# Performance work log

Measured on AMD Instinct MI355X. Metric: run time of the kernel, lower is better.

## Reference

```python
import jax, jax.numpy as jnp
import numpy as np

B, H, K, E = 8, 256, 256, 128
VOCAB, FVOCAB = 30000, 1000


def setup_inputs() -> dict:
    key = jax.random.key(0)
    k1, k2, k3, k4, k5, k6 = jax.random.split(key, 6)
    key_emb = jax.random.normal(k2, (VOCAB, E), dtype=jnp.float32)
    value_emb = jax.random.normal(k3, (FVOCAB, E), dtype=jnp.float32)
    # padding_idx=0 rows are zero
    key_emb = key_emb.at[0].set(0.0)
    value_emb = value_emb.at[0].set(0.0)
    return {
        "hidden": jax.random.normal(k1, (B, H, E), dtype=jnp.float32),
        "key_emb": key_emb,
        "value_emb": value_emb,
        "key_seq": jax.random.randint(k4, (B, K), 0, VOCAB, dtype=jnp.int64) if jax.config.jax_enable_x64 else jax.random.randint(k4, (B, K), 0, VOCAB).astype(jnp.int32),
        "value_seq": jax.random.randint(k5, (B, H, K), 0, FVOCAB).astype(jnp.int32),
        "mask_matrix": jax.random.randint(k6, (B, H, K), 0, 2).astype(jnp.int32),
    }


def reference(hidden, key_emb, value_emb, key_seq, value_seq, mask_matrix):
    scale = jnp.asarray(np.power(E, 0.5), dtype=jnp.float32)
    # embedding gathers (padding_idx=0 -> zero row, enforced in setup)
    k = key_emb[key_seq]            # [B, K, E]
    v = value_emb[value_seq]        # [B, H, K, E]
    # masked exp-normalize attention (manual, not softmax: no max-subtract)
    u = jnp.einsum('bhe,bke->bhk', hidden, k) / scale   # [B, H, K]
    delta = jnp.exp(u) * mask_matrix.astype(jnp.float32)
    p = delta / (jnp.sum(delta, axis=2, keepdims=True) + 1e-10)  # [B, H, K]
    # attention-weighted value aggregation
    o = jnp.einsum('bhk,bhke->bhe', p, v)               # [B, H, E]
    # nonzero-count averaging over H
    aspect_len = jnp.sum(o != 0, axis=1).astype(jnp.float32)     # [B, E]
    avg_o = jnp.sum(o, axis=1) / aspect_len                      # [B, E]
    return avg_o
```

## Files before the change

kernel.cpp:

```cpp
#include <hip/hip_runtime.h>
#include <math.h>

#define BB 8
#define HH 256
#define KK 256
#define EE 128
#define HJ 4
#define NBLK (BB * HH / HJ)
#define NBIN 1024

template <int CTRL, int RM>
__device__ __forceinline__ float dpp_add(float x) {
    int d = __builtin_amdgcn_update_dpp(0, __float_as_int(x), CTRL, RM, 0xf, true);
    return x + __int_as_float(d);
}
__device__ __forceinline__ float dpp_reduce_half(float x) {
    x = dpp_add<0x111, 0xf>(x);
    x = dpp_add<0x112, 0xf>(x);
    x = dpp_add<0x114, 0xf>(x);
    x = dpp_add<0x118, 0xf>(x);
    x = dpp_add<0x142, 0xa>(x);
    return x;
}
__device__ __forceinline__ float dpp_reduce_wave(float x) {
    x = dpp_reduce_half(x);
    x = dpp_add<0x143, 0xc>(x);
    return x;
}

__global__ __launch_bounds__(256) void kvmn_attn_hist(
    const float* __restrict__ hidden,
    const float* __restrict__ key_emb,
    const int*   __restrict__ key_seq,
    const int*   __restrict__ value_seq,
    const int*   __restrict__ mask,
    float* __restrict__ part_hist,
    int*   __restrict__ c_part)
{
    __shared__ float sh_u[HJ][KK];
    __shared__ float hist[NBIN];
    __shared__ float fslot[HJ][4];
    __shared__ int   islot[HJ][4];

    const int bid  = blockIdx.x;
    const int b    = bid >> 6;
    const int h0   = (bid & 63) * HJ;
    const int tid  = threadIdx.x;
    const int w    = tid >> 6;
    const int lane = tid & 63;
    const int half = lane >> 5;
    const int sub  = lane & 31;

    const int ksreg = key_seq[b * KK + tid];

    float4 h4[HJ];
    #pragma unroll
    for (int j = 0; j < HJ; ++j)
        h4[j] = *(const float4*)&hidden[(size_t)(b * HH + h0 + j) * EE + sub * 4];

    *(float4*)&hist[tid * 4] = make_float4(0.f, 0.f, 0.f, 0.f);

    const float inv_scale = 0.08838834764831845f;

    #pragma unroll 8
    for (int i = 0; i < 32; ++i) {
        const int    row = __shfl(ksreg, half * 32 + i, 64);
        const float4 kv  = *(const float4*)&key_emb[(size_t)row * EE + sub * 4];
        const int    k2  = w * 64 + half * 32 + i;
        #pragma unroll
        for (int j = 0; j < HJ; ++j) {
            float part = kv.x * h4[j].x + kv.y * h4[j].y + kv.z * h4[j].z + kv.w * h4[j].w;
            part = dpp_reduce_half(part);
            if (sub == 31) sh_u[j][k2] = part * inv_scale;
        }
    }
    __syncthreads();

    float d[HJ];
    int   vs[HJ];
    #pragma unroll
    for (int j = 0; j < HJ; ++j) {
        const size_t idx = (size_t)(b * HH + h0 + j) * KK + tid;
        const int m = mask[idx];
        vs[j] = value_seq[idx];
        d[j]  = expf(sh_u[j][tid]) * (float)m;
        const float s = dpp_reduce_wave(d[j]);
        if (lane == 63) fslot[j][w] = s;
        const int any = __any(m != 0 && vs[j] != 0);
        if (lane == 0) islot[j][w] = any ? 1 : 0;
    }
    __syncthreads();

    #pragma unroll
    for (int j = 0; j < HJ; ++j) {
        const float denom = fslot[j][0] + fslot[j][1] + fslot[j][2] + fslot[j][3];
        const float p = d[j] * (1.0f / (denom + 1e-10f));
        atomicAdd(&hist[vs[j]], p);
    }
    if (tid == 0) {
        int c = 0;
        #pragma unroll
        for (int j = 0; j < HJ; ++j)
            c += (islot[j][0] | islot[j][1] | islot[j][2] | islot[j][3]);
        c_part[bid] = c;
    }
    __syncthreads();

    *(float4*)&part_hist[(size_t)bid * NBIN + tid * 4] = *(float4*)&hist[tid * 4];
}

__global__ __launch_bounds__(512) void kvmn_finalize(
    const float* __restrict__ part_hist,
    const int*   __restrict__ c_part,
    const float* __restrict__ value_emb,
    float* __restrict__ out)
{
    __shared__ float H[NBIN];
    __shared__ float gs[4][EE];
    __shared__ int   csh[64];
    __shared__ float cval;

    const int b   = blockIdx.x;
    const int tid = threadIdx.x;

    float2 acc2 = make_float2(0.f, 0.f);
    #pragma unroll 8
    for (int i = 0; i < 64; ++i) {
        const float2 v = *(const float2*)&part_hist[(size_t)(b * 64 + i) * NBIN + tid * 2];
        acc2.x += v.x;
        acc2.y += v.y;
    }
    *(float2*)&H[tid * 2] = acc2;
    if (tid < 64) csh[tid] = c_part[b * 64 + tid];
    __syncthreads();
    if (tid == 0) {
        int c = 0;
        #pragma unroll
        for (int i = 0; i < 64; ++i) c += csh[i];
        cval = (float)c;
    }

    const int e  = tid & 127;
    const int qt = tid >> 7;
    float acc = 0.f;
    const int bin0 = qt * 250;
    #pragma unroll 5
    for (int bin = bin0; bin < bin0 + 250; ++bin)
        acc += H[bin] * value_emb[(size_t)bin * EE + e];
    gs[qt][e] = acc;
    __syncthreads();
    if (tid < 128)
        out[b * EE + tid] = (gs[0][tid] + gs[1][tid] + gs[2][tid] + gs[3][tid]) / cval;
}

extern "C" void kernel_launch(void* const* d_in, const int* in_sizes, int n_in,
                              void* d_out, int out_size, void* d_ws, size_t ws_size,
                              hipStream_t stream) {
    const float* hidden    = (const float*)d_in[0];
    const float* key_emb   = (const float*)d_in[1];
    const float* value_emb = (const float*)d_in[2];
    const int*   key_seq   = (const int*)d_in[3];
    const int*   value_seq = (const int*)d_in[4];
    const int*   mask      = (const int*)d_in[5];

    float* part_hist = (float*)d_ws;
    int*   c_part    = (int*)((char*)d_ws + (size_t)NBLK * NBIN * 4);

    kvmn_attn_hist<<<NBLK, 256, 0, stream>>>(hidden, key_emb, key_seq,
                                             value_seq, mask, part_hist, c_part);
    kvmn_finalize<<<BB, 512, 0, stream>>>(part_hist, c_part, value_emb, (float*)d_out);
    (void)in_sizes; (void)n_in; (void)out_size; (void)ws_size;
}
```

Baseline: 115.5 us.

## Merge attention and finalize into one cooperative kernel with parallel reduction

Replaces the two-kernel pipeline with a single cooperative kernel of 1024 blocks, each handling 2 heads instead of 4. Grid syncs separate the phases. The histogram reduction and value-embedding projection are spread over 512 blocks, each taking a 16-bin chunk, instead of running on only 8 blocks. A final phase sums the partial outputs per batch. This targets the serial finalize tail and the launch gap between kernels. In exchange it adds two grid-wide barriers, doubles the partial-histogram traffic to 4 MB, and needs all blocks co-resident.

```diff
diff --git a/kernel.cpp b/kernel.cpp
--- a/kernel.cpp
+++ b/kernel.cpp
@@ -1,13 +1,18 @@
 #include <hip/hip_runtime.h>
+#include <hip/hip_cooperative_groups.h>
 #include <math.h>
+
+namespace cg = cooperative_groups;
 
 #define BB 8
 #define HH 256
 #define KK 256
 #define EE 128
-#define HJ 4
-#define NBLK (BB * HH / HJ)
 #define NBIN 1024
+#define GRID 1024
+#define BPB 128
+#define CHUNK 16
+#define NCH (NBIN / CHUNK)
 
 template <int CTRL, int RM>
 __device__ __forceinline__ float dpp_add(float x) {
@@ -28,129 +33,163 @@
     return x;
 }
 
-__global__ __launch_bounds__(256) void kvmn_attn_hist(
+__global__ __launch_bounds__(256, 4) void kvmn_coop(
     const float* __restrict__ hidden,
     const float* __restrict__ key_emb,
+    const float* __restrict__ value_emb,
     const int*   __restrict__ key_seq,
     const int*   __restrict__ value_seq,
     const int*   __restrict__ mask,
     float* __restrict__ part_hist,
-    int*   __restrict__ c_part)
+    float* __restrict__ partial_out,
+    int*   __restrict__ c_part,
+    float* __restrict__ out)
 {
-    __shared__ float sh_u[HJ][KK];
+    __shared__ float sh_u[2][KK];
     __shared__ float hist[NBIN];
-    __shared__ float fslot[HJ][4];
-    __shared__ int   islot[HJ][4];
+    __shared__ float fslot[2][4];
+    __shared__ int   islot[2][4];
+    __shared__ float red[CHUNK][17];
+    __shared__ float Hc[CHUNK];
+    __shared__ float gs[2][EE];
+    __shared__ int   sh_c[256];
+    __shared__ float sh_cf;
+
+    cg::grid_group grid = cg::this_grid();
 
     const int bid  = blockIdx.x;
-    const int b    = bid >> 6;
-    const int h0   = (bid & 63) * HJ;
     const int tid  = threadIdx.x;
     const int w    = tid >> 6;
     const int lane = tid & 63;
     const int half = lane >> 5;
     const int sub  = lane & 31;
 
-    const int ksreg = key_seq[b * KK + tid];
-
-    float4 h4[HJ];
-    #pragma unroll
-    for (int j = 0; j < HJ; ++j)
-        h4[j] = *(const float4*)&hidden[(size_t)(b * HH + h0 + j) * EE + sub * 4];
-
-    *(float4*)&hist[tid * 4] = make_float4(0.f, 0.f, 0.f, 0.f);
-
-    const float inv_scale = 0.08838834764831845f;
-
-    #pragma unroll 8
-    for (int i = 0; i < 32; ++i) {
-        const int    row = __shfl(ksreg, half * 32 + i, 64);
-        const float4 kv  = *(const float4*)&key_emb[(size_t)row * EE + sub * 4];
-        const int    k2  = w * 64 + half * 32 + i;
-        #pragma unroll
-        for (int j = 0; j < HJ; ++j) {
-            float part = kv.x * h4[j].x + kv.y * h4[j].y + kv.z * h4[j].z + kv.w * h4[j].w;
-            part = dpp_reduce_half(part);
-            if (sub == 31) sh_u[j][k2] = part * inv_scale;
-        }
+    {
+        const int b  = bid >> 7;
+        const int h0 = (bid * 2) & 255;
+
+        const int ksreg = key_seq[b * KK + tid];
+
+        float4 h4[2];
+        #pragma unroll
+        for (int j = 0; j < 2; ++j)
+            h4[j] = *(const float4*)&hidden[((size_t)b * HH + h0 + j) * EE + sub * 4];
+
+        *(float4*)&hist[tid * 4] = make_float4(0.f, 0.f, 0.f, 0.f);
+
+        const float inv_scale = 0.08838834764831845f;
+
+        #pragma unroll 8
+        for (int i = 0; i < 32; ++i) {
+            const int    row = __shfl(ksreg, half * 32 + i, 64);
+            const float4 kv  = *(const float4*)&key_emb[(size_t)row * EE + sub * 4];
+            const int    k2  = w * 64 + half * 32 + i;
+            float p0 = kv.x * h4[0].x + kv.y * h4[0].y + kv.z * h4[0].z + kv.w * h4[0].w;
+            float p1 = kv.x * h4[1].x + kv.y * h4[1].y + kv.z * h4[1].z + kv.w * h4[1].w;
+            p0 = dpp_reduce_half(p0);
+            p1 = dpp_reduce_half(p1);
+            if (sub == 31) {
+                sh_u[0][k2] = p0 * inv_scale;
+                sh_u[1][k2] = p1 * inv_scale;
+            }
+        }
+        __syncthreads();
+
+        float d[2];
+        int   vs[2];
+        #pragma unroll
+        for (int j = 0; j < 2; ++j) {
+            const size_t idx = ((size_t)b * HH + h0 + j) * KK + tid;
+            const int m = mask[idx];
+            vs[j] = value_seq[idx];
+            d[j]  = expf(sh_u[j][tid]) * (float)m;
+            const float s = dpp_reduce_wave(d[j]);
+            if (lane == 63) fslot[j][w] = s;
+            const unsigned long long bal = __ballot(m != 0 && vs[j] != 0);
+            if (lane == 0) islot[j][w] = (bal != 0ull) ? 1 : 0;
+        }
+        __syncthreads();
+
+        #pragma unroll
+        for (int j = 0; j < 2; ++j) {
+            const float denom = fslot[j][0] + fslot[j][1] + fslot[j][2] + fslot[j][3];
+            const float p = d[j] * (1.0f / (denom + 1e-10f));
+            atomicAdd(&hist[vs[j]], p);
+        }
+        if (tid == 0) {
+            const int f0 = islot[0][0] | islot[0][1] | islot[0][2] | islot[0][3];
+            const int f1 = islot[1][0] | islot[1][1] | islot[1][2] | islot[1][3];
+            c_part[bid] = f0 + f1;
+        }
+        __syncthreads();
+
+        *(float4*)&part_hist[(size_t)bid * NBIN + tid * 4] = *(float4*)&hist[tid * 4];
     }
-    __syncthreads();
-
-    float d[HJ];
-    int   vs[HJ];
-    #pragma unroll
-    for (int j = 0; j < HJ; ++j) {
-        const size_t idx = (size_t)(b * HH + h0 + j) * KK + tid;
-        const int m = mask[idx];
-        vs[j] = value_seq[idx];
-        d[j]  = expf(sh_u[j][tid]) * (float)m;
-        const float s = dpp_reduce_wave(d[j]);
-        if (lane == 63) fslot[j][w] = s;
-        const int any = __any(m != 0 && vs[j] != 0);
-        if (lane == 0) islot[j][w] = any ? 1 : 0;
+
+    __threadfence();
+    grid.sync();
+
+    if (bid < BB * NCH) {
+        const int b    = bid >> 6;
+        const int j    = bid & (NCH - 1);
+        const int bin0 = j * CHUNK;
+
+        const int bin = tid & 15;
+        const int rg  = tid >> 4;
+        float s = 0.0f;
+        const float* basep = part_hist + (size_t)(b * BPB + rg * 8) * NBIN + bin0 + bin;
+        #pragma unroll
+        for (int r = 0; r < 8; ++r)
+            s += basep[(size_t)r * NBIN];
+        red[bin][rg] = s;
+        __syncthreads();
+        if (tid < CHUNK) {
+            float t2 = 0.0f;
+            #pragma unroll
+            for (int g = 0; g < 16; ++g) t2 += red[tid][g];
+            Hc[tid] = t2;
+        }
+        __syncthreads();
+
+        const int e  = tid & 127;
+        const int hf = tid >> 7;
+        float acc = 0.0f;
+        #pragma unroll
+        for (int i = 0; i < 8; ++i) {
+            const int gb = bin0 + hf * 8 + i;
+            if (gb < 1000)
+                acc += Hc[hf * 8 + i] * value_emb[(size_t)gb * EE + e];
+        }
+        gs[hf][e] = acc;
+        __syncthreads();
+        if (tid < EE)
+            partial_out[((size_t)b * NCH + j) * EE + tid] = gs[0][tid] + gs[1][tid];
     }
-    __syncthreads();
-
-    #pragma unroll
-    for (int j = 0; j < HJ; ++j) {
-        const float denom = fslot[j][0] + fslot[j][1] + fslot[j][2] + fslot[j][3];
-        const float p = d[j] * (1.0f / (denom + 1e-10f));
-        atomicAdd(&hist[vs[j]], p);
+
+    __threadfence();
+    grid.sync();
+
+    if (bid < BB) {
+        const int b  = bid;
+        const int e  = tid & 127;
+        const int hf = tid >> 7;
+
+        float acc = 0.0f;
+        #pragma unroll 8
+        for (int q = 0; q < 32; ++q)
+            acc += partial_out[((size_t)b * NCH + hf * 32 + q) * EE + e];
+        gs[hf][e] = acc;
+        sh_c[tid] = (tid < BPB) ? c_part[b * BPB + tid] : 0;
+        __syncthreads();
+        if (tid == 0) {
+            int c = 0;
+            for (int i = 0; i < BPB; ++i) c += sh_c[i];
+            sh_cf = (float)c;
+        }
+        __syncthreads();
+        if (tid < EE)
+            out[b * EE + tid] = (gs[0][tid] + gs[1][tid]) / sh_cf;
     }
-    if (tid == 0) {
-        int c = 0;
-        #pragma unroll
-        for (int j = 0; j < HJ; ++j)
-            c += (islot[j][0] | islot[j][1] | islot[j][2] | islot[j][3]);
-        c_part[bid] = c;
-    }
-    __syncthreads();
-
-    *(float4*)&part_hist[(size_t)bid * NBIN + tid * 4] = *(float4*)&hist[tid * 4];
-}
-
-__global__ __launch_bounds__(512) void kvmn_finalize(
-    const float* __restrict__ part_hist,
-    const int*   __restrict__ c_part,
-    const float* __restrict__ value_emb,
-    float* __restrict__ out)
-{
-    __shared__ float H[NBIN];
-    __shared__ float gs[4][EE];
-    __shared__ int   csh[64];
-    __shared__ float cval;
-
-    const int b   = blockIdx.x;
-    const int tid = threadIdx.x;
-
-    float2 acc2 = make_float2(0.f, 0.f);
-    #pragma unroll 8
-    for (int i = 0; i < 64; ++i) {
-        const float2 v = *(const float2*)&part_hist[(size_t)(b * 64 + i) * NBIN + tid * 2];
-        acc2.x += v.x;
-        acc2.y += v.y;
-    }
-    *(float2*)&H[tid * 2] = acc2;
-    if (tid < 64) csh[tid] = c_part[b * 64 + tid];
-    __syncthreads();
-    if (tid == 0) {
-        int c = 0;
-        #pragma unroll
-        for (int i = 0; i < 64; ++i) c += csh[i];
-        cval = (float)c;
-    }
-
-    const int e  = tid & 127;
-    const int qt = tid >> 7;
-    float acc = 0.f;
-    const int bin0 = qt * 250;
-    #pragma unroll 5
-    for (int bin = bin0; bin < bin0 + 250; ++bin)
-        acc += H[bin] * value_emb[(size_t)bin * EE + e];
-    gs[qt][e] = acc;
-    __syncthreads();
-    if (tid < 128)
-        out[b * EE + tid] = (gs[0][tid] + gs[1][tid] + gs[2][tid] + gs[3][tid]) / cval;
 }
 
 extern "C" void kernel_launch(void* const* d_in, const int* in_sizes, int n_in,
@@ -163,11 +202,18 @@
     const int*   value_seq = (const int*)d_in[4];
     const int*   mask      = (const int*)d_in[5];
 
-    float* part_hist = (float*)d_ws;
-    int*   c_part    = (int*)((char*)d_ws + (size_t)NBLK * NBIN * 4);
-
-    kvmn_attn_hist<<<NBLK, 256, 0, stream>>>(hidden, key_emb, key_seq,
-                                             value_seq, mask, part_hist, c_part);
-    kvmn_finalize<<<BB, 512, 0, stream>>>(part_hist, c_part, value_emb, (float*)d_out);
+    char* ws = (char*)d_ws;
+    float* part_hist   = (float*)ws;
+    float* partial_out = (float*)(ws + (4u << 20));
+    int*   c_part      = (int*)  (ws + (4u << 20) + (256u << 10));
+    float* outp        = (float*)d_out;
+
+    void* args[] = {
+        (void*)&hidden, (void*)&key_emb, (void*)&value_emb,
+        (void*)&key_seq, (void*)&value_seq, (void*)&mask,
+        (void*)&part_hist, (void*)&partial_out, (void*)&c_part, (void*)&outp
+    };
+    hipLaunchCooperativeKernel((const void*)kvmn_coop, dim3(GRID), dim3(256),
+                               args, 0, stream);
     (void)in_sizes; (void)n_in; (void)out_size; (void)ws_size;
 }
```

Result: slower. 418.3 us (+262.2%).

## Double heads per block and split finalize across bin chunks with atomic ticket

Applied to the files above, without the earlier changes.

The attention kernel now handles 8 heads per block, which halves the number of partial histograms to 256 per batch-slice and to 32 per batch. The finalize step moves from 8 large blocks to 64 blocks, each covering one 128-bin chunk of the value table. Each block atomically adds its partial output into a workspace, and the last-arriving block, found through a ticket counter, divides by the nonzero count. This aims to cut the serial histogram reduction and GEMV cost in finalize by spreading it over more CUs. In exchange it adds atomics and fences, and the first kernel carries more registers per thread.

```diff
diff --git a/kernel.cpp b/kernel.cpp
--- a/kernel.cpp
+++ b/kernel.cpp
@@ -5,9 +5,10 @@
 #define HH 256
 #define KK 256
 #define EE 128
-#define HJ 4
-#define NBLK (BB * HH / HJ)
 #define NBIN 1024
+#define HJ 8
+#define BPB (HH / HJ)
+#define NB1 (BB * BPB)
 
 template <int CTRL, int RM>
 __device__ __forceinline__ float dpp_add(float x) {
@@ -28,14 +29,16 @@
     return x;
 }
 
-__global__ __launch_bounds__(256) void kvmn_attn_hist(
+__global__ __launch_bounds__(256) void kvmn_attn(
     const float* __restrict__ hidden,
     const float* __restrict__ key_emb,
     const int*   __restrict__ key_seq,
     const int*   __restrict__ value_seq,
     const int*   __restrict__ mask,
     float* __restrict__ part_hist,
-    int*   __restrict__ c_part)
+    int*   __restrict__ c_part,
+    float* __restrict__ sum_ws,
+    int*   __restrict__ ticket)
 {
     __shared__ float sh_u[HJ][KK];
     __shared__ float hist[NBIN];
@@ -43,26 +46,32 @@
     __shared__ int   islot[HJ][4];
 
     const int bid  = blockIdx.x;
-    const int b    = bid >> 6;
-    const int h0   = (bid & 63) * HJ;
+    const int b    = bid >> 5;
+    const int h0   = (bid & 31) * HJ;
     const int tid  = threadIdx.x;
     const int w    = tid >> 6;
     const int lane = tid & 63;
     const int half = lane >> 5;
     const int sub  = lane & 31;
 
+    if (bid == 0) {
+        if (tid < BB * EE / 4)
+            *(float4*)&sum_ws[tid * 4] = make_float4(0.f, 0.f, 0.f, 0.f);
+        if (tid < BB) ticket[tid] = 0;
+    }
+
     const int ksreg = key_seq[b * KK + tid];
 
     float4 h4[HJ];
     #pragma unroll
     for (int j = 0; j < HJ; ++j)
-        h4[j] = *(const float4*)&hidden[(size_t)(b * HH + h0 + j) * EE + sub * 4];
+        h4[j] = *(const float4*)&hidden[((size_t)b * HH + h0 + j) * EE + sub * 4];
 
     *(float4*)&hist[tid * 4] = make_float4(0.f, 0.f, 0.f, 0.f);
 
     const float inv_scale = 0.08838834764831845f;
 
-    #pragma unroll 8
+    #pragma unroll 4
     for (int i = 0; i < 32; ++i) {
         const int    row = __shfl(ksreg, half * 32 + i, 64);
         const float4 kv  = *(const float4*)&key_emb[(size_t)row * EE + sub * 4];
@@ -80,14 +89,14 @@
     int   vs[HJ];
     #pragma unroll
     for (int j = 0; j < HJ; ++j) {
-        const size_t idx = (size_t)(b * HH + h0 + j) * KK + tid;
+        const size_t idx = ((size_t)b * HH + h0 + j) * KK + tid;
         const int m = mask[idx];
         vs[j] = value_seq[idx];
         d[j]  = expf(sh_u[j][tid]) * (float)m;
         const float s = dpp_reduce_wave(d[j]);
         if (lane == 63) fslot[j][w] = s;
-        const int any = __any(m != 0 && vs[j] != 0);
-        if (lane == 0) islot[j][w] = any ? 1 : 0;
+        const unsigned long long bal = __ballot(m != 0 && vs[j] != 0);
+        if (lane == 0) islot[j][w] = (bal != 0ull) ? 1 : 0;
     }
     __syncthreads();
 
@@ -109,48 +118,69 @@
     *(float4*)&part_hist[(size_t)bid * NBIN + tid * 4] = *(float4*)&hist[tid * 4];
 }
 
-__global__ __launch_bounds__(512) void kvmn_finalize(
+__global__ __launch_bounds__(256) void kvmn_hgemm(
     const float* __restrict__ part_hist,
     const int*   __restrict__ c_part,
     const float* __restrict__ value_emb,
+    float* __restrict__ sum_ws,
+    int*   __restrict__ ticket,
     float* __restrict__ out)
 {
-    __shared__ float H[NBIN];
-    __shared__ float gs[4][EE];
-    __shared__ int   csh[64];
-    __shared__ float cval;
-
-    const int b   = blockIdx.x;
+    __shared__ float Hsh[2][128];
+    __shared__ float gs[2][EE];
+    __shared__ bool  isLast;
+    __shared__ float sh_cf;
+
+    const int bid = blockIdx.x;
+    const int b   = bid >> 3;
+    const int ch  = bid & 7;
     const int tid = threadIdx.x;
-
-    float2 acc2 = make_float2(0.f, 0.f);
+    const int bin = tid & 127;
+    const int rh  = tid >> 7;
+
+    float s = 0.0f;
+    const float* base = part_hist + ((size_t)(b * BPB) + rh * 16) * NBIN + ch * 128 + bin;
+    #pragma unroll 8
+    for (int r = 0; r < 16; ++r)
+        s += base[(size_t)r * NBIN];
+    Hsh[rh][bin] = s;
+    __syncthreads();
+    if (tid < 128) Hsh[0][tid] += Hsh[1][tid];
+    __syncthreads();
+
+    const int e  = tid & 127;
+    const int hf = tid >> 7;
+    float acc = 0.0f;
     #pragma unroll 8
     for (int i = 0; i < 64; ++i) {
-        const float2 v = *(const float2*)&part_hist[(size_t)(b * 64 + i) * NBIN + tid * 2];
-        acc2.x += v.x;
-        acc2.y += v.y;
-    }
-    *(float2*)&H[tid * 2] = acc2;
-    if (tid < 64) csh[tid] = c_part[b * 64 + tid];
+        const int gb = ch * 128 + hf * 64 + i;
+        if (gb < 1000)
+            acc += Hsh[0][hf * 64 + i] * value_emb[(size_t)gb * EE + e];
+    }
+    gs[hf][e] = acc;
+    __syncthreads();
+
+    if (tid < 128) atomicAdd(&sum_ws[b * EE + tid], gs[0][tid] + gs[1][tid]);
+    __threadfence();
     __syncthreads();
     if (tid == 0) {
-        int c = 0;
-        #pragma unroll
-        for (int i = 0; i < 64; ++i) c += csh[i];
-        cval = (float)c;
-    }
-
-    const int e  = tid & 127;
-    const int qt = tid >> 7;
-    float acc = 0.f;
-    const int bin0 = qt * 250;
-    #pragma unroll 5
-    for (int bin = bin0; bin < bin0 + 250; ++bin)
-        acc += H[bin] * value_emb[(size_t)bin * EE + e];
-    gs[qt][e] = acc;
-    __syncthreads();
-    if (tid < 128)
-        out[b * EE + tid] = (gs[0][tid] + gs[1][tid] + gs[2][tid] + gs[3][tid]) / cval;
+        const int old = atomicAdd(&ticket[b], 1);
+        isLast = (old == 7);
+    }
+    __syncthreads();
+
+    if (isLast) {
+        __threadfence();
+        if (tid == 0) {
+            int c = 0;
+            #pragma unroll
+            for (int r = 0; r < BPB; ++r) c += c_part[b * BPB + r];
+            sh_cf = (float)c;
+        }
+        __syncthreads();
+        if (tid < EE)
+            out[b * EE + tid] = sum_ws[b * EE + tid] / sh_cf;
+    }
 }
 
 extern "C" void kernel_launch(void* const* d_in, const int* in_sizes, int n_in,
@@ -163,11 +193,15 @@
     const int*   value_seq = (const int*)d_in[4];
     const int*   mask      = (const int*)d_in[5];
 
-    float* part_hist = (float*)d_ws;
-    int*   c_part    = (int*)((char*)d_ws + (size_t)NBLK * NBIN * 4);
-
-    kvmn_attn_hist<<<NBLK, 256, 0, stream>>>(hidden, key_emb, key_seq,
-                                             value_seq, mask, part_hist, c_part);
-    kvmn_finalize<<<BB, 512, 0, stream>>>(part_hist, c_part, value_emb, (float*)d_out);
+    char* ws = (char*)d_ws;
+    float* part_hist = (float*)ws;
+    int*   c_part    = (int*)  (ws + (1u << 20));
+    float* sum_ws    = (float*)(ws + (1u << 20) + 1024);
+    int*   ticket    = (int*)  (ws + (1u << 20) + 1024 + 4096);
+
+    kvmn_attn <<<NB1, 256, 0, stream>>>(hidden, key_emb, key_seq, value_seq, mask,
+                                        part_hist, c_part, sum_ws, ticket);
+    kvmn_hgemm<<<64, 256, 0, stream>>>(part_hist, c_part, value_emb,
+                                       sum_ws, ticket, (float*)d_out);
     (void)in_sizes; (void)n_in; (void)out_size; (void)ws_size;
 }
```

Measured after the change: 125.5 us. 1.09x slower.
